# Kernel optimization log

Measured on AMD Instinct MI355X. Metric: run time of the kernel, lower is better.

The kernel has to match this reference:

```python
import jax, jax.numpy as jnp
import numpy as np

NUM_HEADS = 16  # CLIP ViT-L num_attention_heads


def setup_inputs() -> dict:
    key = jax.random.key(0)
    ks = jax.random.split(key, 11)
    B, T, E = 16, 577, 1024
    d = {
        "hidden_states": jax.random.normal(ks[0], (B, T, E), jnp.float32),
        # token 'size' from prior merging steps; sizes are >= 1 in practice
        "size": jax.random.uniform(ks[1], (B, T), jnp.float32) + 1.0,
        "wq": jax.random.normal(ks[2], (E, E), jnp.float32) * (E ** -0.5),
        "bq": jax.random.normal(ks[3], (E,), jnp.float32) * 0.02,
        "wk": jax.random.normal(ks[4], (E, E), jnp.float32) * (E ** -0.5),
        "bk": jax.random.normal(ks[5], (E,), jnp.float32) * 0.02,
        "wv": jax.random.normal(ks[6], (E, E), jnp.float32) * (E ** -0.5),
        "bv": jax.random.normal(ks[7], (E,), jnp.float32) * 0.02,
        "wo": jax.random.normal(ks[8], (E, E), jnp.float32) * (E ** -0.5),
        "bo": jax.random.normal(ks[9], (E,), jnp.float32) * 0.02,
    }
    return d


def reference(hidden_states, size, wq, bq, wk, bk, wv, bv, wo, bo):
    B, T, E = hidden_states.shape
    H = NUM_HEADS
    D = E // H
    scale = D ** -0.5

    # torch nn.Linear: y = x @ W.T + b
    q = (hidden_states @ wq.T + bq) * scale
    k = hidden_states @ wk.T + bk
    v = hidden_states @ wv.T + bv

    def split_heads(x):  # [B,T,E] -> [B,H,T,D]
        return x.reshape(B, T, H, D).transpose(0, 2, 1, 3)

    qh, kh, vh = split_heads(q), split_heads(k), split_heads(v)

    # raw logits (before size bias), [B,H,T,T]
    attn_logits = jnp.einsum("bhtd,bhsd->bhts", qh, kh)

    # att_score: mean over the flattened bsz*num_heads dim, on raw logits
    att_score = attn_logits.mean(axis=(0, 1))  # [T,T]

    # additive log-size bias over keys
    attn_logits = attn_logits + jnp.log(size)[:, None, None, :]

    probs = jax.nn.softmax(attn_logits, axis=-1)  # dropout p=0 / eval
    out = jnp.einsum("bhts,bhsd->bhtd", probs, vh)
    out = out.transpose(0, 2, 1, 3).reshape(B, T, E)
    attn_output = out @ wo.T + bo

    # mean over heads of key states: [B,T,D]
    mean_keys = kh.mean(axis=1)

    return attn_output, mean_keys, att_score
```

## Files before the change

kernel.cpp:

```cpp
#include <hip/hip_runtime.h>
#include <hip/hip_bf16.h>
#include <math.h>

typedef __attribute__((ext_vector_type(8))) short s16x8;
typedef __attribute__((ext_vector_type(4))) short s16x4;
typedef __attribute__((ext_vector_type(4))) float f32x4;
typedef __attribute__((ext_vector_type(8))) __bf16 bf16x8;

#define MFMA16(a, b, c) __builtin_amdgcn_mfma_f32_16x16x32_bf16( \
    __builtin_bit_cast(bf16x8, (a)), __builtin_bit_cast(bf16x8, (b)), (c), 0, 0, 0)

__device__ __forceinline__ short f2b(float f) {
    __bf16 h = (__bf16)f;
    return __builtin_bit_cast(short, h);
}
__device__ __forceinline__ float b2f(short b) {
    union { unsigned u; float f; } x;
    x.u = ((unsigned)(unsigned short)b) << 16;
    return x.f;
}

__device__ __forceinline__ void gload16(const void* g, void* l) {
    __builtin_amdgcn_global_load_lds(
        (const __attribute__((address_space(1))) unsigned int*)g,
        (__attribute__((address_space(3))) unsigned int*)l, 16, 0, 0);
}

__global__ void k_f32_to_bf16(const float* __restrict__ in, short* __restrict__ out, long n) {
    long i = ((long)blockIdx.x * blockDim.x + threadIdx.x) * 4;
    long stride = (long)gridDim.x * blockDim.x * 4;
    for (; i < n; i += stride) {
        float4 v = *(const float4*)(in + i);
        s16x4 o = { f2b(v.x), f2b(v.y), f2b(v.z), f2b(v.w) };
        *(s16x4*)(out + i) = o;
    }
}

__global__ void k_wconv4(const float* __restrict__ w0, const float* __restrict__ w1,
                         const float* __restrict__ w2, const float* __restrict__ w3,
                         short* __restrict__ out, long n) {
    int wsel = blockIdx.y;
    const float* src = (wsel == 0) ? w0 : (wsel == 1) ? w1 : (wsel == 2) ? w2 : w3;
    short* dst = out + (long)wsel * n;
    long i = ((long)blockIdx.x * blockDim.x + threadIdx.x) * 4;
    if (i >= n) return;
    float4 v = *(const float4*)(src + i);
    s16x4 o = { f2b(v.x), f2b(v.y), f2b(v.z), f2b(v.w) };
    *(s16x4*)(dst + i) = o;
}

__global__ void k_sizepad(const float* __restrict__ size, float* __restrict__ out,
                          int B, int T, int SP) {
    int i = blockIdx.x * blockDim.x + threadIdx.x;
    if (i >= B * SP) return;
    int b = i / SP, s = i % SP;
    out[i] = (s < T) ? size[b * T + s] : 0.f;
}

template<bool ROUTE>
__global__ __launch_bounds__(512, 4) void k_gemm8w(
    const short* __restrict__ A, const short* __restrict__ Bw,
    const float* __restrict__ bb0, const float* __restrict__ bb1, const float* __restrict__ bb2,
    short* __restrict__ o0, short* __restrict__ o1, short* __restrict__ o2,
    float* __restrict__ Cf, int M, int N, int K, int Ntiles, float alpha0) {

    __shared__ short As[128 * 64];
    __shared__ short Bs[128 * 64];

    int nwg = gridDim.x, orig = blockIdx.x;
    int qq = nwg >> 3, rr = nwg & 7;
    int xcd = orig & 7, pos = orig >> 3;
    int wg = (xcd < rr ? xcd * (qq + 1) : rr * (qq + 1) + (xcd - rr) * qq) + pos;
    int bx = wg % Ntiles, by = wg / Ntiles;
    int row0 = by * 128, col0 = bx * 128;

    int tid = threadIdx.x;
    int lane = tid & 63, wave = tid >> 6;
    int wr = wave >> 1, wc = wave & 1;
    int lr = lane & 15, lg = lane >> 4;

    f32x4 acc[2][4];
    #pragma unroll
    for (int i = 0; i < 2; i++)
        #pragma unroll
        for (int j = 0; j < 4; j++)
            #pragma unroll
            for (int q = 0; q < 4; q++) acc[i][j][q] = 0.f;

    for (int k0 = 0; k0 < K; k0 += 64) {
        __syncthreads();
        #pragma unroll
        for (int jj = 0; jj < 2; ++jj) {
            int ch = tid + jj * 512;
            int r = ch >> 3;
            int cby = ((ch & 7) * 16) ^ ((r & 7) << 4);
            int ra = row0 + r; ra = ra < M ? ra : M - 1;
            gload16((const char*)(A + (long)ra * K + k0) + cby, &As[ch * 8]);
            int rb = col0 + r; rb = rb < N ? rb : N - 1;
            gload16((const char*)(Bw + (long)rb * K + k0) + cby, &Bs[ch * 8]);
        }
        __syncthreads();
        #pragma unroll
        for (int ks = 0; ks < 2; ++ks) {
            s16x8 af[2];
            #pragma unroll
            for (int i = 0; i < 2; ++i) {
                int r = wr * 32 + i * 16 + lr;
                af[i] = *(const s16x8*)((const char*)As + r * 128 +
                        (((ks << 6) + (lg << 4)) ^ ((r & 7) << 4)));
            }
            #pragma unroll
            for (int j = 0; j < 4; ++j) {
                int r = wc * 64 + j * 16 + lr;
                s16x8 bfr = *(const s16x8*)((const char*)Bs + r * 128 +
                            (((ks << 6) + (lg << 4)) ^ ((r & 7) << 4)));
                acc[0][j] = MFMA16(af[0], bfr, acc[0][j]);
                acc[1][j] = MFMA16(af[1], bfr, acc[1][j]);
            }
        }
    }

    #pragma unroll
    for (int i = 0; i < 2; i++) {
        int grow0 = row0 + wr * 32 + i * 16 + lg * 4;
        #pragma unroll
        for (int j = 0; j < 4; j++) {
            int gc = col0 + wc * 64 + j * 16 + lr;
            if (gc >= N) continue;
            if (ROUTE) {
                int which = gc >> 10, lc = gc & 1023;
                float bias = (which == 0 ? bb0 : which == 1 ? bb1 : bb2)[lc];
                float alpha = (which == 0) ? alpha0 : 1.0f;
                short* op = (which == 0 ? o0 : which == 1 ? o1 : o2);
                #pragma unroll
                for (int q = 0; q < 4; ++q) {
                    int r2 = grow0 + q;
                    if (r2 < M) op[(long)r2 * 1024 + lc] = f2b((acc[i][j][q] + bias) * alpha);
                }
            } else {
                float bias = bb0[gc];
                #pragma unroll
                for (int q = 0; q < 4; ++q) {
                    int r2 = grow0 + q;
                    if (r2 < M) Cf[(long)r2 * N + gc] = acc[i][j][q] + bias;
                }
            }
        }
    }
}

__device__ __forceinline__ void core32(
    const short* __restrict__ A, const short* __restrict__ Bw,
    int M, int N, int K, int row0, int col0,
    short* AS, short* BS,
    f32x4 acc[4][4]) {
    int tid = threadIdx.x;
    int lane = tid & 63, wave = tid >> 6;
    int wr = wave >> 1, wc = wave & 1;
    int lr = lane & 15, lg = lane >> 4;

    const char* ga[2]; const char* gb[2]; int ldo[2];
    #pragma unroll
    for (int j = 0; j < 2; ++j) {
        int ch = j * 256 + wave * 64 + lane;
        int r = ch >> 2, slot = ch & 3;
        int cby = (slot << 4) ^ (((r >> 1) & 3) << 4);
        int ra = row0 + r; ra = ra < M ? ra : M - 1;
        int rb = col0 + r; rb = rb < N ? rb : N - 1;
        ga[j] = (const char*)(A + (long)ra * K) + cby;
        gb[j] = (const char*)(Bw + (long)rb * K) + cby;
        ldo[j] = ch * 8;
    }
    #pragma unroll
    for (int i = 0; i < 4; i++)
        #pragma unroll
        for (int j = 0; j < 4; j++)
            #pragma unroll
            for (int q = 0; q < 4; q++) acc[i][j][q] = 0.f;

    #pragma unroll
    for (int j = 0; j < 2; ++j) {
        gload16(ga[j], AS + ldo[j]);
        gload16(gb[j], BS + ldo[j]);
        ga[j] += 64; gb[j] += 64;
    }

    int nt = K >> 5;
    for (int t = 0; t < nt; ++t) {
        int cur = t & 1;
        asm volatile("s_waitcnt vmcnt(0)" ::: "memory");
        __builtin_amdgcn_s_barrier();
        if (t + 1 < nt) {
            short* Ad = AS + (cur ^ 1) * 4096;
            short* Bd = BS + (cur ^ 1) * 4096;
            #pragma unroll
            for (int j = 0; j < 2; ++j) {
                gload16(ga[j], Ad + ldo[j]);
                gload16(gb[j], Bd + ldo[j]);
                ga[j] += 64; gb[j] += 64;
            }
        }
        const short* Ab2 = AS + cur * 4096;
        const short* Bb2 = BS + cur * 4096;
        s16x8 af[4], bfr[4];
        #pragma unroll
        for (int i = 0; i < 4; ++i) {
            int r = wr * 64 + i * 16 + lr;
            af[i] = *(const s16x8*)((const char*)Ab2 + r * 64 +
                    ((lg << 4) ^ (((r >> 1) & 3) << 4)));
        }
        #pragma unroll
        for (int j = 0; j < 4; ++j) {
            int r = wc * 64 + j * 16 + lr;
            bfr[j] = *(const s16x8*)((const char*)Bb2 + r * 64 +
                     ((lg << 4) ^ (((r >> 1) & 3) << 4)));
        }
        __builtin_amdgcn_s_setprio(1);
        #pragma unroll
        for (int i = 0; i < 4; ++i)
            #pragma unroll
            for (int j = 0; j < 4; ++j)
                acc[i][j] = MFMA16(af[i], bfr[j], acc[i][j]);
        __builtin_amdgcn_s_setprio(0);
    }
}

__global__ __launch_bounds__(256) void k_proj32(
    const short* __restrict__ A, const short* __restrict__ Bw,
    const float* __restrict__ bias, float* __restrict__ Cf,
    int M, int N, int K, int Ntiles) {
    __shared__ short AS[2][128 * 32];
    __shared__ short BS[2][128 * 32];

    int nwg = gridDim.x, orig = blockIdx.x;
    int qq = nwg >> 3, rr = nwg & 7;
    int xcd = orig & 7, pos = orig >> 3;
    int wg = (xcd < rr ? xcd * (qq + 1) : rr * (qq + 1) + (xcd - rr) * qq) + pos;
    int bx = wg % Ntiles, by = wg / Ntiles;
    int row0 = by * 128, col0 = bx * 128;

    int tid = threadIdx.x;
    int lane = tid & 63, wave = tid >> 6;
    int wr = wave >> 1, wc = wave & 1;
    int lr = lane & 15, lg = lane >> 4;

    f32x4 acc[4][4];
    core32(A, Bw, M, N, K, row0, col0, &AS[0][0], &BS[0][0], acc);

    #pragma unroll
    for (int i = 0; i < 4; i++) {
        int grow0 = row0 + wr * 64 + i * 16 + lg * 4;
        #pragma unroll
        for (int j = 0; j < 4; j++) {
            int gc = col0 + wc * 64 + j * 16 + lr;
            if (gc >= N) continue;
            float bv = bias[gc];
            #pragma unroll
            for (int q = 0; q < 4; ++q) {
                int r2 = grow0 + q;
                if (r2 < M) Cf[(long)r2 * N + gc] = acc[i][j][q] + bv;
            }
        }
    }
}

__global__ __launch_bounds__(256) void k_att(
    const short* __restrict__ q, const short* __restrict__ k,
    float* __restrict__ attp, int T, int E) {
    __shared__ short AS[2][128 * 32];
    __shared__ short BS[2][128 * 32];
    int z = blockIdx.z;
    const short* Ab = q + (long)z * T * E;
    const short* Bb = k + (long)z * T * E;
    float* Cf = attp + (long)z * T * T;
    int row0 = blockIdx.y * 128, col0 = blockIdx.x * 128;

    int tid = threadIdx.x;
    int lane = tid & 63, wave = tid >> 6;
    int wr = wave >> 1, wc = wave & 1;
    int lr = lane & 15, lg = lane >> 4;

    f32x4 acc[4][4];
    core32(Ab, Bb, T, T, E, row0, col0, &AS[0][0], &BS[0][0], acc);

    #pragma unroll
    for (int i = 0; i < 4; i++) {
        int rbase = row0 + wr * 64 + i * 16 + lg * 4;
        #pragma unroll
        for (int j = 0; j < 4; j++) {
            int c = col0 + wc * 64 + j * 16 + lr;
            if (c >= T) continue;
            #pragma unroll
            for (int q2 = 0; q2 < 4; q2++) {
                int r = rbase + q2;
                if (r >= T) continue;
                Cf[(long)r * T + c] = acc[i][j][q2];
            }
        }
    }
}

__global__ void k_mean_keys8(const short* __restrict__ Kb, float* __restrict__ out, int BT) {
    int i = blockIdx.x * blockDim.x + threadIdx.x;
    if (i >= BT * 8) return;
    int bt = i >> 3, d0 = (i & 7) * 8;
    const short* p = Kb + (long)bt * 1024 + d0;
    float s[8] = {0.f, 0.f, 0.f, 0.f, 0.f, 0.f, 0.f, 0.f};
    #pragma unroll
    for (int h = 0; h < 16; ++h) {
        s16x8 v = *(const s16x8*)(p + h * 64);
        #pragma unroll
        for (int j = 0; j < 8; ++j) s[j] += b2f(v[j]);
    }
    float4 o0 = {s[0] * 0.0625f, s[1] * 0.0625f, s[2] * 0.0625f, s[3] * 0.0625f};
    float4 o1 = {s[4] * 0.0625f, s[5] * 0.0625f, s[6] * 0.0625f, s[7] * 0.0625f};
    *(float4*)(out + (long)bt * 64 + d0) = o0;
    *(float4*)(out + (long)bt * 64 + d0 + 4) = o1;
}

__global__ void k_att_reduce(const float* __restrict__ part, float* __restrict__ out,
                             int n, int nb, long stride) {
    int i = blockIdx.x * blockDim.x + threadIdx.x;
    if (i >= n) return;
    float s = 0.f;
    for (int b = 0; b < nb; ++b) s += part[(long)b * stride + i];
    out[i] = s * 0.002707606174062286f;
}

__global__ __launch_bounds__(256) void k_vtrans(const short* __restrict__ v, short* __restrict__ vt,
                                                const float* __restrict__ szp,
                                                int B, int T, int H, int TP, int SP) {
    int b = blockIdx.z, h = blockIdx.y, t0 = blockIdx.x * 64;
    __shared__ short Vs[64][68];
    __shared__ float Szs[64];
    int tid = threadIdx.x;
    if (tid < 64) Szs[tid] = szp[b * SP + t0 + tid];
    for (int c = tid; c < 512; c += 256) {
        int r = c >> 3, m = c & 7;
        s16x8 val = {0,0,0,0,0,0,0,0};
        if (t0 + r < T) val = *(const s16x8*)(v + ((long)(b * T + t0 + r)) * (H * 64) + h * 64 + m * 8);
        *(s16x8*)&Vs[r][m * 8] = val;
    }
    __syncthreads();
    for (int c = tid; c < 512; c += 256) {
        int d = c >> 3, mw = c & 7;
        s16x8 o;
        #pragma unroll
        for (int j = 0; j < 8; j++) o[j] = f2b(b2f(Vs[mw * 8 + j][d]) * Szs[mw * 8 + j]);
        *(s16x8*)(vt + ((long)((b * H + h) * 64 + d)) * TP + t0 + mw * 8) = o;
    }
}

__global__ __launch_bounds__(256) void k_flash(
    const short* __restrict__ Q, const short* __restrict__ Kb, const short* __restrict__ VT,
    const float* __restrict__ szp, short* __restrict__ Ctx,
    int B, int T, int E, int H, int SP, int TP, int NTQ) {
    int nwg = gridDim.x;
    int cpx = nwg >> 3;
    int wg = (blockIdx.x & 7) * cpx + (blockIdx.x >> 3);
    int tq = wg % NTQ, h = (wg / NTQ) % H, b = wg / (NTQ * H);
    int t0 = tq * 64;

    __shared__ short Ks[64][68];
    __shared__ short Vt[80][68];
    __shared__ short Ps[4][16][68];
    int tid = threadIdx.x, wid = tid >> 6, lane = tid & 63;
    int lr = lane & 15, lg = lane >> 4;

    for (int c = tid; c < 15 * 68; c += 256) Vt[65 + c / 68][c % 68] = 0;

    s16x8 aqf[2];
    {
        int t = t0 + wid * 16 + lr; t = t < T ? t : T - 1;
        #pragma unroll
        for (int ks = 0; ks < 2; ++ks)
            aqf[ks] = *(const s16x8*)(Q + ((long)b * T + t) * E + h * 64 + ks * 32 + lg * 8);
    }

    const short* kb  = Kb + (long)b * T * E + h * 64;
    const short* vtb = VT + ((long)(b * H + h)) * 64 * TP;

    int c0 = tid, c1 = tid + 256;
    int r0 = c0 >> 3, m0 = c0 & 7, r1 = c1 >> 3, m1 = c1 & 7;
    s16x8 kreg0, kreg1, vreg0, vreg1;
    float szreg = 0.f;

    {
        int s = r0; s = s < T ? s : T - 1;
        kreg0 = *(const s16x8*)(kb + (long)s * E + m0 * 8);
        s = r1; s = s < T ? s : T - 1;
        kreg1 = *(const s16x8*)(kb + (long)s * E + m1 * 8);
        vreg0 = *(const s16x8*)(vtb + (long)r0 * TP + 0 + m0 * 8);
        vreg1 = *(const s16x8*)(vtb + (long)r1 * TP + 0 + m1 * 8);
        if (tid < 64) szreg = szp[b * SP + 0 + tid];
    }

    float mreg[4];
    f32x4 o[5];
    #pragma unroll
    for (int q = 0; q < 4; q++) mreg[q] = -INFINITY;
    #pragma unroll
    for (int jd = 0; jd < 5; jd++)
        #pragma unroll
        for (int q = 0; q < 4; q++) o[jd][q] = 0.f;

    for (int s0 = 0; s0 < T; s0 += 64) {
        *(s16x8*)&Ks[r0][m0 * 8] = kreg0;
        *(s16x8*)&Ks[r1][m1 * 8] = kreg1;
        *(s16x8*)&Vt[r0][m0 * 8] = vreg0;
        *(s16x8*)&Vt[r1][m1 * 8] = vreg1;
        if (tid < 64) Vt[64][tid] = f2b(szreg);
        __syncthreads();

        if (s0 + 64 < T) {
            int sn = s0 + 64;
            int s = sn + r0; s = s < T ? s : T - 1;
            kreg0 = *(const s16x8*)(kb + (long)s * E + m0 * 8);
            s = sn + r1; s = s < T ? s : T - 1;
            kreg1 = *(const s16x8*)(kb + (long)s * E + m1 * 8);
            vreg0 = *(const s16x8*)(vtb + (long)r0 * TP + sn + m0 * 8);
            vreg1 = *(const s16x8*)(vtb + (long)r1 * TP + sn + m1 * 8);
            if (tid < 64) szreg = szp[b * SP + sn + tid];
        }

        f32x4 sf[4];
        #pragma unroll
        for (int j = 0; j < 4; j++)
            #pragma unroll
            for (int q = 0; q < 4; q++) sf[j][q] = 0.f;
        __builtin_amdgcn_s_setprio(1);
        #pragma unroll
        for (int ks = 0; ks < 2; ++ks)
            #pragma unroll
            for (int j = 0; j < 4; j++) {
                s16x8 bk = *(const s16x8*)&Ks[j * 16 + lr][ks * 32 + lg * 8];
                sf[j] = MFMA16(aqf[ks], bk, sf[j]);
            }
        __builtin_amdgcn_s_setprio(0);

        float tmax[4];
        #pragma unroll
        for (int q = 0; q < 4; q++)
            tmax[q] = fmaxf(fmaxf(sf[0][q], sf[1][q]), fmaxf(sf[2][q], sf[3][q]));
        int ok = 1;
        #pragma unroll
        for (int q = 0; q < 4; q++) ok &= (tmax[q] <= mreg[q] + 11.0f) ? 1 : 0;
        if (!__all(ok)) {
            #pragma unroll
            for (int q = 0; q < 4; q++) {
                #pragma unroll
                for (int msk = 1; msk < 16; msk <<= 1)
                    tmax[q] = fmaxf(tmax[q], __shfl_xor(tmax[q], msk));
                float mn = fmaxf(mreg[q], tmax[q]);
                float al = exp2f(mreg[q] - mn);
                mreg[q] = mn;
                #pragma unroll
                for (int jd = 0; jd < 5; jd++) o[jd][q] *= al;
            }
        }
        #pragma unroll
        for (int j = 0; j < 4; j++)
            #pragma unroll
            for (int q = 0; q < 4; q++)
                Ps[wid][lg * 4 + q][j * 16 + lr] = f2b(exp2f(sf[j][q] - mreg[q]));

        __builtin_amdgcn_s_setprio(1);
        #pragma unroll
        for (int ks = 0; ks < 2; ++ks) {
            s16x8 ap = *(const s16x8*)&Ps[wid][lr][ks * 32 + lg * 8];
            #pragma unroll
            for (int jd = 0; jd < 5; jd++) {
                s16x8 bv = *(const s16x8*)&Vt[jd * 16 + lr][ks * 32 + lg * 8];
                o[jd] = MFMA16(ap, bv, o[jd]);
            }
        }
        __builtin_amdgcn_s_setprio(0);
        __syncthreads();
    }

    short* cb = Ctx + ((long)b * T + t0) * E + h * 64;
    #pragma unroll
    for (int q = 0; q < 4; q++) {
        float s = __shfl(o[4][q], lane & 48);
        int t = wid * 16 + lg * 4 + q;
        if (t0 + t >= T) continue;
        float inv = 1.f / s;
        #pragma unroll
        for (int jd = 0; jd < 4; jd++)
            cb[(long)t * E + jd * 16 + lr] = f2b(o[jd][q] * inv);
    }
}

extern "C" void kernel_launch(void* const* d_in, const int* in_sizes, int n_in,
                              void* d_out, int out_size, void* d_ws, size_t ws_size,
                              hipStream_t stream) {
    (void)in_sizes; (void)n_in; (void)out_size; (void)ws_size;
    const int B = 16, T = 577, E = 1024, H = 16;
    const int SP = 640, TP = 640;
    const float* hs   = (const float*)d_in[0];
    const float* size = (const float*)d_in[1];
    const float* wq   = (const float*)d_in[2];
    const float* bq   = (const float*)d_in[3];
    const float* wk   = (const float*)d_in[4];
    const float* bk   = (const float*)d_in[5];
    const float* wv   = (const float*)d_in[6];
    const float* bv   = (const float*)d_in[7];
    const float* wo   = (const float*)d_in[8];
    const float* bo   = (const float*)d_in[9];

    float* out_attn = (float*)d_out;
    float* out_mk   = out_attn + (long)B * T * E;
    float* out_as   = out_mk + (long)B * T * 64;

    long nBTE = (long)B * T * E;
    long nEE  = (long)E * E;
    char* ws = (char*)d_ws;
    short* hs_b  = (short*)ws; ws += nBTE * 2;
    short* wq_b  = (short*)ws; ws += nEE * 2;
    short* wk_b  = (short*)ws; ws += nEE * 2;
    short* wv_b  = (short*)ws; ws += nEE * 2;
    short* wo_b  = (short*)ws; ws += nEE * 2;
    short* q_b   = (short*)ws; ws += nBTE * 2;
    short* k_b   = (short*)ws; ws += nBTE * 2;
    short* v_b   = (short*)ws; ws += nBTE * 2;
    short* ctx_b = (short*)ws; ws += nBTE * 2;
    float* szpad = (float*)ws; ws += (long)B * SP * 4;
    float* att_p = (float*)ws; ws += (long)B * T * T * 4;
    short* vt = (short*)att_p;

    k_f32_to_bf16<<<2048, 256, 0, stream>>>(hs, hs_b, nBTE);
    {
        dim3 gw((nEE / 4 + 255) / 256, 4);
        k_wconv4<<<gw, 256, 0, stream>>>(wq, wk, wv, wo, wq_b, nEE);
    }
    k_sizepad<<<(B * SP + 255) / 256, 256, 0, stream>>>(size, szpad, B, T, SP);

    int M = B * T;
    {
        int Mtiles = (M + 127) / 128, Ntiles = 3072 / 128;
        k_gemm8w<true><<<Mtiles * Ntiles, 512, 0, stream>>>(
            hs_b, wq_b, bq, bk, bv, q_b, k_b, v_b, nullptr, M, 3072, E, Ntiles,
            0.18033688011112042f);
    }

    dim3 g_att((T + 127) / 128, (T + 127) / 128, B);
    k_att<<<g_att, dim3(256), 0, stream>>>(q_b, k_b, att_p, T, E);
    k_att_reduce<<<((T * T) + 255) / 256, 256, 0, stream>>>(att_p, out_as, T * T, B, (long)T * T);

    dim3 g_vt((T + 63) / 64, H, B);
    k_vtrans<<<g_vt, dim3(256), 0, stream>>>(v_b, vt, szpad, B, T, H, TP, SP);

    k_mean_keys8<<<((B * T * 8) + 255) / 256, 256, 0, stream>>>(k_b, out_mk, B * T);

    const int NTQ = (T + 63) / 64;
    int nfl = NTQ * H * B;
    k_flash<<<nfl, dim3(256), 0, stream>>>(q_b, k_b, vt, szpad, ctx_b, B, T, E, H, SP, TP, NTQ);

    {
        int Mtiles = (M + 127) / 128, Ntiles = 1024 / 128;
        k_proj32<<<Mtiles * Ntiles, 256, 0, stream>>>(
            ctx_b, wo_b, bo, out_attn, M, 1024, E, Ntiles);
    }
}
```

Measured before the change: 275.0 us.

## Load flash K/V tiles straight into swizzled LDS via global_load_lds

The register-staged prefetch of K and V^T tiles in the flash attention kernel is replaced by direct global-to-LDS loads (global_load_lds). The padded LDS arrays become unpadded ones whose 16-byte chunks are XOR-swizzled by row, with the same XOR applied on the global source address and on the MFMA operand reads. The goal is to cut VGPR staging and LDS store instructions and to avoid bank conflicts without padding. In exchange, each tile is now loaded and waited on (vmcnt(0)) inside the same iteration, so the previous overlap of next-tile global loads with compute is lost.

```diff
diff --git a/kernel.cpp b/kernel.cpp
--- a/kernel.cpp
+++ b/kernel.cpp
@@ -361,13 +361,13 @@
     int tq = wg % NTQ, h = (wg / NTQ) % H, b = wg / (NTQ * H);
     int t0 = tq * 64;
 
-    __shared__ short Ks[64][68];
-    __shared__ short Vt[80][68];
+    __shared__ short KsL[64 * 64];
+    __shared__ short VtL[80 * 64];
     __shared__ short Ps[4][16][68];
     int tid = threadIdx.x, wid = tid >> 6, lane = tid & 63;
     int lr = lane & 15, lg = lane >> 4;
 
-    for (int c = tid; c < 15 * 68; c += 256) Vt[65 + c / 68][c % 68] = 0;
+    for (int c = tid; c < 15 * 64; c += 256) VtL[65 * 64 + c] = 0;
 
     s16x8 aqf[2];
     {
@@ -380,20 +380,11 @@
     const short* kb  = Kb + (long)b * T * E + h * 64;
     const short* vtb = VT + ((long)(b * H + h)) * 64 * TP;
 
-    int c0 = tid, c1 = tid + 256;
-    int r0 = c0 >> 3, m0 = c0 & 7, r1 = c1 >> 3, m1 = c1 & 7;
-    s16x8 kreg0, kreg1, vreg0, vreg1;
-    float szreg = 0.f;
-
-    {
-        int s = r0; s = s < T ? s : T - 1;
-        kreg0 = *(const s16x8*)(kb + (long)s * E + m0 * 8);
-        s = r1; s = s < T ? s : T - 1;
-        kreg1 = *(const s16x8*)(kb + (long)s * E + m1 * 8);
-        vreg0 = *(const s16x8*)(vtb + (long)r0 * TP + 0 + m0 * 8);
-        vreg1 = *(const s16x8*)(vtb + (long)r1 * TP + 0 + m1 * 8);
-        if (tid < 64) szreg = szp[b * SP + 0 + tid];
-    }
+    int ch0 = tid, ch1 = tid + 256;
+    int kr0 = ch0 >> 3, kc0 = ((ch0 & 7) * 16) ^ ((kr0 & 7) << 4);
+    int kr1 = ch1 >> 3, kc1 = ((ch1 & 7) * 16) ^ ((kr1 & 7) << 4);
+
+    float szreg = (tid < 64) ? szp[b * SP + tid] : 0.f;
 
     float mreg[4];
     f32x4 o[5];
@@ -405,23 +396,21 @@
         for (int q = 0; q < 4; q++) o[jd][q] = 0.f;
 
     for (int s0 = 0; s0 < T; s0 += 64) {
-        *(s16x8*)&Ks[r0][m0 * 8] = kreg0;
-        *(s16x8*)&Ks[r1][m1 * 8] = kreg1;
-        *(s16x8*)&Vt[r0][m0 * 8] = vreg0;
-        *(s16x8*)&Vt[r1][m1 * 8] = vreg1;
-        if (tid < 64) Vt[64][tid] = f2b(szreg);
         __syncthreads();
-
-        if (s0 + 64 < T) {
-            int sn = s0 + 64;
-            int s = sn + r0; s = s < T ? s : T - 1;
-            kreg0 = *(const s16x8*)(kb + (long)s * E + m0 * 8);
-            s = sn + r1; s = s < T ? s : T - 1;
-            kreg1 = *(const s16x8*)(kb + (long)s * E + m1 * 8);
-            vreg0 = *(const s16x8*)(vtb + (long)r0 * TP + sn + m0 * 8);
-            vreg1 = *(const s16x8*)(vtb + (long)r1 * TP + sn + m1 * 8);
-            if (tid < 64) szreg = szp[b * SP + sn + tid];
-        }
+        {
+            int s = s0 + kr0; s = s < T ? s : T - 1;
+            gload16((const char*)(kb + (long)s * E) + kc0, &KsL[ch0 * 8]);
+            s = s0 + kr1; s = s < T ? s : T - 1;
+            gload16((const char*)(kb + (long)s * E) + kc1, &KsL[ch1 * 8]);
+            gload16((const char*)(vtb + (long)kr0 * TP + s0) + kc0, &VtL[ch0 * 8]);
+            gload16((const char*)(vtb + (long)kr1 * TP + s0) + kc1, &VtL[ch1 * 8]);
+        }
+        if (tid < 64) {
+            VtL[64 * 64 + tid] = f2b(szreg);
+            if (s0 + 64 < T) szreg = szp[b * SP + s0 + 64 + tid];
+        }
+        asm volatile("s_waitcnt vmcnt(0)" ::: "memory");
+        __syncthreads();
 
         f32x4 sf[4];
         #pragma unroll
@@ -433,7 +422,9 @@
         for (int ks = 0; ks < 2; ++ks)
             #pragma unroll
             for (int j = 0; j < 4; j++) {
-                s16x8 bk = *(const s16x8*)&Ks[j * 16 + lr][ks * 32 + lg * 8];
+                int r = j * 16 + lr;
+                s16x8 bk = *(const s16x8*)((const char*)KsL + r * 128 +
+                           (((ks << 6) + (lg << 4)) ^ ((r & 7) << 4)));
                 sf[j] = MFMA16(aqf[ks], bk, sf[j]);
             }
         __builtin_amdgcn_s_setprio(0);
@@ -470,12 +461,13 @@
             s16x8 ap = *(const s16x8*)&Ps[wid][lr][ks * 32 + lg * 8];
             #pragma unroll
             for (int jd = 0; jd < 5; jd++) {
-                s16x8 bv = *(const s16x8*)&Vt[jd * 16 + lr][ks * 32 + lg * 8];
+                int r = jd * 16 + lr;
+                s16x8 bv = *(const s16x8*)((const char*)VtL + r * 128 +
+                           (((ks << 6) + (lg << 4)) ^ ((r & 7) << 4)));
                 o[jd] = MFMA16(ap, bv, o[jd]);
             }
         }
         __builtin_amdgcn_s_setprio(0);
-        __syncthreads();
     }
 
     short* cb = Ctx + ((long)b * T + t0) * E + h * 64;
```

Result: faster. 264.5 us (-3.8%).
